# Optimization experiments

Hardware: AMD Instinct MI355X
Metric: run time of the kernel (lower is better)

## Reference

```python
import jax, jax.numpy as jnp
import numpy as np
from jax import lax

LATENT_DIM, INPUT_DIM, KERNEL = 16, 3, 3
B, H, W = 64, 128, 128


def make_masks(C, K):
    mid = K // 2
    mask0 = np.ones((C, C, K, K), np.float32)
    mask1 = np.zeros((C, C, K, K), np.float32)
    mask = np.ones((C, C, K, K), np.float32)
    for i in range(C):
        mask0[i, i, mid, mid] = 0.0
        mask1[i, i, mid, mid] = 1.0
        mask[i, :, mid + 1:, :] = 0.0
        mask[i, :i + 1, mid, mid + 1:] = 0.0
        mask[i, i + 1:, mid, mid:] = 0.0
    return jnp.asarray(mask0), jnp.asarray(mask1), jnp.asarray(mask)


def setup_inputs() -> dict:
    key = jax.random.key(0)
    ks = jax.random.split(key, 6)
    L, C, K = LATENT_DIM, INPUT_DIM, KERNEL
    # xavier-normal std for (C,C,K,K) weights: sqrt(2/(fan_in+fan_out)), fan = C*K*K
    xstd = np.sqrt(2.0 / (2 * C * K * K)).astype(np.float32)
    return {
        "x": jax.random.normal(ks[0], (B, C, H, W), jnp.float32),
        "weight1": jax.random.normal(ks[1], (L, C, C, K, K), jnp.float32) * xstd,
        "center1": jax.random.normal(ks[2], (L, C, C, K, K), jnp.float32),
        "bias1": jax.random.normal(ks[3], (L, C), jnp.float32),
        "weight2": jax.random.normal(ks[4], (L, C, C, K, K), jnp.float32) * xstd,
        "center2": jax.random.normal(ks[5], (L, C, C, K, K), jnp.float32),
        "res": jnp.ones((1,), jnp.float32),
    }


def _conv(x, w, groups=1):
    return lax.conv_general_dilated(
        x, w, window_strides=(1, 1), padding=((1, 1), (1, 1)),
        dimension_numbers=("NCHW", "OIHW", "NCHW"), feature_group_count=groups)


def reference(x, weight1, center1, bias1, weight2, center2, res):
    L, C, K = LATENT_DIM, INPUT_DIM, KERNEL
    mask0, mask1, mask = make_masks(C, K)
    # masked weights, built for all latents at once: [L, C, C, K, K]
    w1 = (weight1 * mask0 + jax.nn.softplus(center1) * mask1) * mask
    w2 = (weight2 * mask0 + jax.nn.softplus(center2) * mask1) * mask
    # stage 1: single conv producing all L latents -> [B, L*C, H, W]
    h = _conv(x, w1.reshape(L * C, C, K, K)) + bias1.reshape(1, L * C, 1, 1)
    h = jax.nn.elu(h)
    # stage 2: grouped conv, one group per latent (no bias in original)
    h2 = _conv(h, w2.reshape(L * C, C, K, K), groups=L)  # [B, L*C, H, W]
    out = h2.reshape(B, L, C, H, W).mean(axis=1)
    gate = (res > 0).astype(x.dtype)
    return out + res * gate * x
```

## Files before the change

kernel.cpp:

```cpp
#include <hip/hip_runtime.h>
#include <hip/hip_bf16.h>
#include <math.h>


typedef short bf16x8 __attribute__((ext_vector_type(8)));
typedef short bf16x4 __attribute__((ext_vector_type(4)));
typedef float f32x4  __attribute__((ext_vector_type(4)));

namespace {
constexpr int NC = 3, NH = 128, NW = 128;
constexpr int TS = 16;
constexpr int XRow = 20, XCol = 20;
constexpr int NPX = 306;
constexpr int NT  = 20;
constexpr int W2OFF = 1536;
constexpr int WTN   = 1536 + 4096;
}

__device__ __forceinline__ float softplusf(float v) {
    return v > 20.f ? v : log1pf(expf(v));
}
__device__ __forceinline__ unsigned short f2bf(float v) {
    __hip_bfloat16 h = __float2bfloat16(v);
    return *reinterpret_cast<unsigned short*>(&h);
}

__global__ void prep_weights(const float* __restrict__ w1, const float* __restrict__ c1,
                             const float* __restrict__ b1,
                             const float* __restrict__ w2, const float* __restrict__ c2,
                             unsigned short* __restrict__ tab) {
    int e = blockIdx.x * 256 + threadIdx.x;
    if (e >= WTN) return;
    float v = 0.f;
    if (e < W2OFF) {
        int f = e >> 9, lane = (e >> 3) & 63, j = e & 7;
        int m = lane & 15, q = lane >> 4;
        int k = q * 8 + j;
        int ky = k >> 4, kx = (k >> 2) & 3, chin = k & 3;
        int ch = f * 16 + m;
        if (ch < 48) {
            if (kx < 3 && chin < 3) {
                int l = ch / 3, i = ch - l * 3;
                bool live = (ky == 0) || (kx == 0) || (kx == 1 && chin <= i);
                if (live) {
                    int g = ((l * 3 + i) * 3 + chin) * 9 + ky * 3 + kx;
                    v = (i == chin && ky == 1 && kx == 1) ? softplusf(c1[g]) : w1[g];
                }
            } else if (chin == 3 && ky == 0 && kx == 0) {
                v = b1[ch];
            } else if (chin == 3 && ky == 0 && kx == 1) {
                float b  = b1[ch];
                float bh = __uint_as_float(((unsigned)f2bf(b)) << 16);
                v = b - bh;
            }
        }
    } else {
        int e2 = e - W2OFF;
        int mf = e2 >> 9, lane = (e2 >> 3) & 63, j = e2 & 7;
        int n = lane & 15, q = lane >> 4;
        int k = mf * 32 + q * 8 + j;
        if (n < 3 && k < 240) {
            int c  = k / 48, ch = k - c * 48;
            int ky = (c >= 3) ? 1 : 0, kx = c - 3 * ky;
            int l = ch / 3, jj = ch - l * 3;
            bool live = (ky == 0) || (kx == 0) || (kx == 1 && jj <= n);
            if (live) {
                int g = ((l * 3 + n) * 3 + jj) * 9 + ky * 3 + kx;
                v = (n == jj && ky == 1 && kx == 1) ? softplusf(c2[g]) : w2[g];
            }
        }
    }
    tab[e] = f2bf(v);
}

__global__ __launch_bounds__(256, 5) void fused_mfma(
    const float* __restrict__ x,
    const float* __restrict__ res, const unsigned short* __restrict__ tab,
    float* __restrict__ out)
{
    __shared__ __align__(16) unsigned short xsb[XRow * XCol * 4];
    __shared__ __align__(16) unsigned short hsb[6 * NPX * 8];

    const int tid  = threadIdx.x;
    const int b    = blockIdx.z;
    const int py0  = blockIdx.y * TS;
    const int px0  = blockIdx.x * TS;
    const int lane = tid & 63;
    const int wv   = tid >> 6;
    const int n    = lane & 15;
    const int q    = lane >> 4;

    const float* xb = x + b * NC * NH * NW;
    #pragma unroll
    for (int it = 0; it < 2; ++it) {
        unsigned p = tid + it * 256;
        if (p < XRow * XCol) {
            unsigned r = p / XCol, c = p - r * XCol;
            int gy = (int)(py0 - 2 + r), gx = (int)(px0 - 2 + c);
            bool ok = ((unsigned)gy < NH) && ((unsigned)gx < NW);
            const float* sp = xb + gy * NW + gx;
            float v0 = ok ? sp[0]           : 0.f;
            float v1 = ok ? sp[NH * NW]     : 0.f;
            float v2 = ok ? sp[2 * NH * NW] : 0.f;
            float one = 1.0f;
            unsigned ua, ub;
            asm("v_cvt_pk_bf16_f32 %0, %1, %2" : "=v"(ua) : "v"(v0), "v"(v1));
            asm("v_cvt_pk_bf16_f32 %0, %1, %2" : "=v"(ub) : "v"(v2), "v"(one));
            uint2 st; st.x = ua; st.y = ub;
            *(uint2*)(xsb + p * 4) = st;
        }
    }

    float rg; { float rv = res[0]; rg = rv > 0.f ? rv : 0.f; }

    bf16x8 a1f0 = *(const bf16x8*)(tab + (0 * 64 + lane) * 8);
    bf16x8 a1f1 = *(const bf16x8*)(tab + (1 * 64 + lane) * 8);
    bf16x8 a1f2 = *(const bf16x8*)(tab + (2 * 64 + lane) * 8);

    __syncthreads();

    constexpr int OSTR = NPX * 8;
    #pragma unroll 1
    for (int t = wv; t < NT; t += 4) {
        unsigned p  = t * 16 + n;
        unsigned pr = p / 18, pc = p - pr * 18;
        const unsigned short* bp =
            xsb + ((pr + (q >> 1)) * XCol + pc + ((q & 1) << 1)) * 4;
        bf16x4 lo = *(const bf16x4*)bp;
        bf16x4 hi = *(const bf16x4*)(bp + 4);
        bf16x8 bf;
        #pragma unroll
        for (int j = 0; j < 4; ++j) { bf[j] = lo[j]; bf[4 + j] = hi[j]; }
        f32x4 z = {0.f, 0.f, 0.f, 0.f};
        f32x4 cc0 = __builtin_amdgcn_mfma_f32_16x16x32_bf16(a1f0, bf, z, 0, 0, 0);
        f32x4 cc1 = __builtin_amdgcn_mfma_f32_16x16x32_bf16(a1f1, bf, z, 0, 0, 0);
        f32x4 cc2 = __builtin_amdgcn_mfma_f32_16x16x32_bf16(a1f2, bf, z, 0, 0, 0);
        float mk = (((unsigned)(py0 + (int)pr - 1) < NH) &&
                    ((unsigned)(px0 + (int)pc - 1) < NW)) ? 1.f : 0.f;
        if (p < NPX) {
            f32x4 cc[3] = {cc0, cc1, cc2};
            unsigned short* hp = hsb + p * 8 + ((q & 1) << 2);
            #pragma unroll
            for (int f = 0; f < 3; ++f) {
                float e_[4];
                #pragma unroll
                for (int r = 0; r < 4; ++r) {
                    float t_ = cc[f][r];
                    e_[r] = (t_ > 0.f ? t_ : __expf(t_) - 1.f) * mk;
                }
                unsigned ua, ub;
                asm("v_cvt_pk_bf16_f32 %0, %1, %2" : "=v"(ua) : "v"(e_[0]), "v"(e_[1]));
                asm("v_cvt_pk_bf16_f32 %0, %1, %2" : "=v"(ub) : "v"(e_[2]), "v"(e_[3]));
                uint2 st; st.x = ua; st.y = ub;
                *(uint2*)(hp + ((q >> 1) + f * 2) * OSTR) = st;
            }
        }
    }

    bf16x8 b2k[8];
    #pragma unroll
    for (int m = 0; m < 8; ++m)
        b2k[m] = *(const bf16x8*)(tab + W2OFF + (m * 64 + lane) * 8);

    int dlt[8];
    #pragma unroll
    for (int m = 0; m < 8; ++m) {
        int idx = m * 32 + q * 8;
        int c   = idx / 48;
        int off = idx - c * 48;
        int ky  = (c >= 3) ? 1 : 0, kx = c - 3 * ky;
        dlt[m] = (idx < 240) ? ((off >> 3) * NPX + ky * 18 + kx) * 8 : 0;
    }

    __syncthreads();

    float* ob = out + b * NC * NH * NW;
    #pragma unroll 1
    for (int s = 0; s < 4; ++s) {
        int py = wv + s * 4;
        const unsigned short* hbase = hsb + (py * 18 + n) * 8;
        f32x4 acc[4];
        #pragma unroll
        for (int a = 0; a < 4; ++a) acc[a] = (f32x4){0.f, 0.f, 0.f, 0.f};
        #pragma unroll
        for (int m = 0; m < 8; ++m) {
            bf16x8 af = *(const bf16x8*)(hbase + dlt[m]);
            acc[m & 3] = __builtin_amdgcn_mfma_f32_16x16x32_bf16(af, b2k[m], acc[m & 3], 0, 0, 0);
        }
        if (n < 3) {
            f32x4 t0, t1, sum;
            #pragma unroll
            for (int r = 0; r < 4; ++r) {
                t0[r] = acc[0][r] + acc[1][r];
                t1[r] = acc[2][r] + acc[3][r];
                sum[r] = t0[r] + t1[r];
            }
            int gy = py0 + py;
            const float* xp = xb + n * NH * NW + gy * NW + px0;
            float*       op = ob + n * NH * NW + gy * NW + px0;
            float4 xv = *(const float4*)(xp + q * 4);
            float4 o;
            o.x = sum[0] * (1.f / 16.f) + rg * xv.x;
            o.y = sum[1] * (1.f / 16.f) + rg * xv.y;
            o.z = sum[2] * (1.f / 16.f) + rg * xv.z;
            o.w = sum[3] * (1.f / 16.f) + rg * xv.w;
            *(float4*)(op + q * 4) = o;
        }
    }
}

extern "C" void kernel_launch(void* const* d_in, const int* in_sizes, int n_in,
                              void* d_out, int out_size, void* d_ws, size_t ws_size,
                              hipStream_t stream) {
    (void)in_sizes; (void)n_in; (void)out_size; (void)ws_size;
    const float* x   = (const float*)d_in[0];
    const float* w1  = (const float*)d_in[1];
    const float* c1  = (const float*)d_in[2];
    const float* b1  = (const float*)d_in[3];
    const float* w2  = (const float*)d_in[4];
    const float* c2  = (const float*)d_in[5];
    const float* res = (const float*)d_in[6];
    float* out = (float*)d_out;
    unsigned short* tab = (unsigned short*)d_ws;

    hipLaunchKernelGGL(prep_weights, dim3((WTN + 255) / 256), dim3(256), 0, stream,
                       w1, c1, b1, w2, c2, tab);
    hipLaunchKernelGGL(fused_mfma, dim3(NW / TS, NH / TS, 64), dim3(256), 0, stream,
                       x, res, tab, out);
}
```

Before: 101.8 us.

## Pack 4 output rows x 3 channels into stage-2 MFMA N dimension

Stage 2 changes from four passes per wave (one output row each, only 3 of 16 N columns useful) to one pass that packs 4 rows times 3 channels into 12 of the 16 N columns. The weight table grows to 28 K-slices that encode the row offset, and B fragments are streamed from global memory instead of being held in registers. The aim is to cut wasted MFMA work and the number of LDS A-fragment loads. In exchange it needs more weight-table reads and a larger prep table. A minor change also moves the border mask to a select on the packed bf16 values.

```diff
diff --git a/kernel.cpp b/kernel.cpp
--- a/kernel.cpp
+++ b/kernel.cpp
@@ -14,7 +14,8 @@
 constexpr int NPX = 306;
 constexpr int NT  = 20;
 constexpr int W2OFF = 1536;
-constexpr int WTN   = 1536 + 4096;
+constexpr int NM2   = 28;
+constexpr int WTN   = 1536 + NM2 * 512;
 }
 
 __device__ __forceinline__ float softplusf(float v) {
@@ -56,17 +57,23 @@
         }
     } else {
         int e2 = e - W2OFF;
-        int mf = e2 >> 9, lane = (e2 >> 3) & 63, j = e2 & 7;
+        int mf = e2 >> 9;
+        int lane = (e2 >> 3) & 63, j = e2 & 7;
         int n = lane & 15, q = lane >> 4;
-        int k = mf * 32 + q * 8 + j;
-        if (n < 3 && k < 240) {
-            int c  = k / 48, ch = k - c * 48;
-            int ky = (c >= 3) ? 1 : 0, kx = c - 3 * ky;
-            int l = ch / 3, jj = ch - l * 3;
-            bool live = (ky == 0) || (kx == 0) || (kx == 1 && jj <= n);
-            if (live) {
-                int g = ((l * 3 + n) * 3 + jj) * 9 + ky * 3 + kx;
-                v = (n == jj && ky == 1 && kx == 1) ? softplusf(c2[g]) : w2[g];
+        int p  = mf >> 1, hh = mf & 1;
+        int rho = p / 3, kx = p - rho * 3;
+        int chOct = hh * 4 + q;
+        int ch = n >> 2, dy = n & 3;
+        if (ch < 3 && chOct < 6) {
+            int ch48 = chOct * 8 + j;
+            int l = ch48 / 3, jj = ch48 - l * 3;
+            int ky = rho - dy;
+            if (ky == 0 || ky == 1) {
+                bool live = (ky == 0) || (kx == 0) || (kx == 1 && jj <= ch);
+                if (live) {
+                    int g = ((l * 3 + ch) * 3 + jj) * 9 + ky * 3 + kx;
+                    v = (ch == jj && ky == 1 && kx == 1) ? softplusf(c2[g]) : w2[g];
+                }
             }
         }
     }
@@ -135,8 +142,8 @@
         f32x4 cc0 = __builtin_amdgcn_mfma_f32_16x16x32_bf16(a1f0, bf, z, 0, 0, 0);
         f32x4 cc1 = __builtin_amdgcn_mfma_f32_16x16x32_bf16(a1f1, bf, z, 0, 0, 0);
         f32x4 cc2 = __builtin_amdgcn_mfma_f32_16x16x32_bf16(a1f2, bf, z, 0, 0, 0);
-        float mk = (((unsigned)(py0 + (int)pr - 1) < NH) &&
-                    ((unsigned)(px0 + (int)pc - 1) < NW)) ? 1.f : 0.f;
+        bool mok = (((unsigned)(py0 + (int)pr - 1) < NH) &&
+                    ((unsigned)(px0 + (int)pc - 1) < NW));
         if (p < NPX) {
             f32x4 cc[3] = {cc0, cc1, cc2};
             unsigned short* hp = hsb + p * 8 + ((q & 1) << 2);
@@ -146,58 +153,51 @@
                 #pragma unroll
                 for (int r = 0; r < 4; ++r) {
                     float t_ = cc[f][r];
-                    e_[r] = (t_ > 0.f ? t_ : __expf(t_) - 1.f) * mk;
+                    e_[r] = t_ > 0.f ? t_ : __expf(t_) - 1.f;
                 }
                 unsigned ua, ub;
                 asm("v_cvt_pk_bf16_f32 %0, %1, %2" : "=v"(ua) : "v"(e_[0]), "v"(e_[1]));
                 asm("v_cvt_pk_bf16_f32 %0, %1, %2" : "=v"(ub) : "v"(e_[2]), "v"(e_[3]));
-                uint2 st; st.x = ua; st.y = ub;
+                uint2 st; st.x = mok ? ua : 0u; st.y = mok ? ub : 0u;
                 *(uint2*)(hp + ((q >> 1) + f * 2) * OSTR) = st;
             }
         }
     }
 
-    bf16x8 b2k[8];
+    __syncthreads();
+
+    const unsigned short* vb  = hsb + q * OSTR + (wv * 4 * 18 + n) * 8;
+    const unsigned short* vb1 = (q < 2) ? (vb + 4 * OSTR) : vb;
+
+    f32x4 acc[4];
     #pragma unroll
-    for (int m = 0; m < 8; ++m)
-        b2k[m] = *(const bf16x8*)(tab + W2OFF + (m * 64 + lane) * 8);
-
-    int dlt[8];
+    for (int a = 0; a < 4; ++a) acc[a] = (f32x4){0.f, 0.f, 0.f, 0.f};
+
+    constexpr int P_RHO[14] = {0,0,0,1,1,1,2,2,2,3,3,3,4,4};
+    constexpr int P_KX[14]  = {0,1,2,0,1,2,0,1,2,0,1,2,0,1};
     #pragma unroll
-    for (int m = 0; m < 8; ++m) {
-        int idx = m * 32 + q * 8;
-        int c   = idx / 48;
-        int off = idx - c * 48;
-        int ky  = (c >= 3) ? 1 : 0, kx = c - 3 * ky;
-        dlt[m] = (idx < 240) ? ((off >> 3) * NPX + ky * 18 + kx) * 8 : 0;
-    }
-
-    __syncthreads();
+    for (int m = 0; m < NM2; ++m) {
+        int pp = m >> 1;
+        const unsigned short* ap = (m & 1) ? vb1 : vb;
+        bf16x8 af = *(const bf16x8*)(ap + (P_RHO[pp] * 18 + P_KX[pp]) * 8);
+        bf16x8 bf2 = *(const bf16x8*)(tab + W2OFF + (m * 64 + lane) * 8);
+        acc[m & 3] = __builtin_amdgcn_mfma_f32_16x16x32_bf16(af, bf2, acc[m & 3], 0, 0, 0);
+    }
 
     float* ob = out + b * NC * NH * NW;
-    #pragma unroll 1
-    for (int s = 0; s < 4; ++s) {
-        int py = wv + s * 4;
-        const unsigned short* hbase = hsb + (py * 18 + n) * 8;
-        f32x4 acc[4];
+    {
+        f32x4 t0, t1, sum;
         #pragma unroll
-        for (int a = 0; a < 4; ++a) acc[a] = (f32x4){0.f, 0.f, 0.f, 0.f};
-        #pragma unroll
-        for (int m = 0; m < 8; ++m) {
-            bf16x8 af = *(const bf16x8*)(hbase + dlt[m]);
-            acc[m & 3] = __builtin_amdgcn_mfma_f32_16x16x32_bf16(af, b2k[m], acc[m & 3], 0, 0, 0);
-        }
-        if (n < 3) {
-            f32x4 t0, t1, sum;
-            #pragma unroll
-            for (int r = 0; r < 4; ++r) {
-                t0[r] = acc[0][r] + acc[1][r];
-                t1[r] = acc[2][r] + acc[3][r];
-                sum[r] = t0[r] + t1[r];
-            }
-            int gy = py0 + py;
-            const float* xp = xb + n * NH * NW + gy * NW + px0;
-            float*       op = ob + n * NH * NW + gy * NW + px0;
+        for (int r = 0; r < 4; ++r) {
+            t0[r] = acc[0][r] + acc[1][r];
+            t1[r] = acc[2][r] + acc[3][r];
+            sum[r] = t0[r] + t1[r];
+        }
+        if (n < 12) {
+            int ch = n >> 2, dy = n & 3;
+            int gy = py0 + wv * 4 + dy;
+            const float* xp = xb + ch * NH * NW + gy * NW + px0;
+            float*       op = ob + ch * NH * NW + gy * NW + px0;
             float4 xv = *(const float4*)(xp + q * 4);
             float4 o;
             o.x = sum[0] * (1.f / 16.f) + rg * xv.x;
```

Result: no change. 100.8 us (-1.0%).
